# Performance work log

Measured on AMD Instinct MI355X. Metric: run time of the kernel, lower is better.

## Reference

```python
import jax, jax.numpy as jnp
import numpy as np

NUM_LAYERS = 2

def setup_inputs() -> dict:
    key = jax.random.key(0)
    ks = jax.random.split(key, 10)
    N, E, V, D, G = 50000, 800000, 100000, 128, 64
    node_ids = jax.random.randint(ks[0], (N,), 0, V)
    edge_index = jax.random.randint(ks[1], (2, E), 0, N)
    batch = jnp.sort(jax.random.randint(ks[2], (N,), 0, G))
    embed = jax.random.normal(ks[3], (V, D), dtype=jnp.float32)
    conv_w = jax.random.normal(ks[4], (NUM_LAYERS, D, D), dtype=jnp.float32) * (1.0 / np.sqrt(D))
    w_ih = jax.random.normal(ks[5], (3 * D, D), dtype=jnp.float32) * (1.0 / np.sqrt(D))
    w_hh = jax.random.normal(ks[6], (3 * D, D), dtype=jnp.float32) * (1.0 / np.sqrt(D))
    b_ih = jax.random.normal(ks[7], (3 * D,), dtype=jnp.float32) * 0.01
    b_hh = jax.random.normal(ks[8], (3 * D,), dtype=jnp.float32) * 0.01
    return {"node_ids": node_ids, "edge_index": edge_index, "batch": batch,
            "num_graphs": 64, "embed": embed, "conv_w": conv_w,
            "w_ih": w_ih, "w_hh": w_hh, "b_ih": b_ih, "b_hh": b_hh}


def _gru_cell(x, h, w_ih, w_hh, b_ih, b_hh):
    # torch.nn.GRUCell math; gate order r, z, n
    gi = x @ w_ih.T + b_ih
    gh = h @ w_hh.T + b_hh
    i_r, i_z, i_n = jnp.split(gi, 3, axis=-1)
    h_r, h_z, h_n = jnp.split(gh, 3, axis=-1)
    r = jax.nn.sigmoid(i_r + h_r)
    z = jax.nn.sigmoid(i_z + h_z)
    n = jnp.tanh(i_n + r * h_n)
    return (1.0 - z) * n + z * h


def reference(node_ids, edge_index, batch, num_graphs, embed, conv_w, w_ih, w_hh, b_ih, b_hh):
    N = node_ids.shape[0]
    src, dst = edge_index[0], edge_index[1]
    h = embed[node_ids]  # [N, D]
    for i in range(NUM_LAYERS):
        m = h @ conv_w[i]                                   # [N, D]
        agg = jax.ops.segment_sum(m[src], dst, num_segments=N)  # scatter-add messages
        h = _gru_cell(agg, h, w_ih, w_hh, b_ih, b_hh)
    # global mean pool per graph
    sums = jax.ops.segment_sum(h, batch, num_segments=num_graphs)       # [G, D]
    counts = jax.ops.segment_sum(jnp.ones((N,), h.dtype), batch, num_segments=num_graphs)
    return sums / jnp.maximum(counts, 1.0)[:, None]
```

## Files before the change

kernel.cpp:

```cpp
#include <hip/hip_runtime.h>
#include <hip/hip_bf16.h>


#define DTHREADS 256

typedef __attribute__((ext_vector_type(8))) short bf16x8;
typedef __attribute__((ext_vector_type(4))) float f32x4;

__device__ __forceinline__ float sigf(float x) { return 1.0f / (1.0f + __expf(-x)); }
__device__ __forceinline__ float tanhfast(float x) { return 1.0f - 2.0f / (1.0f + __expf(2.0f * x)); }

__device__ __forceinline__ unsigned short f2bf_rne(float x) {
  unsigned int u = __float_as_uint(x);
  u += 0x7fff + ((u >> 16) & 1);
  return (unsigned short)(u >> 16);
}
__device__ __forceinline__ float bf2f(unsigned int lo16) {
  return __uint_as_float(lo16 << 16);
}

__global__ __launch_bounds__(DTHREADS) void gather_kernel(
    const float* __restrict__ embed, const int* __restrict__ node_ids,
    unsigned short* __restrict__ hb, int N) {
  int idx = blockIdx.x * DTHREADS + threadIdx.x;
  if (idx >= N * 32) return;
  int n = idx >> 5;
  int c = (idx & 31) * 4;
  int v = node_ids[n];
  float4 val = *(const float4*)&embed[(size_t)v * 128 + c];
  unsigned short b[4] = {f2bf_rne(val.x), f2bf_rne(val.y), f2bf_rne(val.z), f2bf_rne(val.w)};
  *(ushort4*)&hb[(size_t)n * 128 + c] = *(ushort4*)b;
}

#define BSHIFT 7
#define BNODES 128

__global__ __launch_bounds__(DTHREADS) void bucket_hist_kernel(
    const int* __restrict__ dst, int* __restrict__ gcnt, int E, int NB) {
  __shared__ int lc[512];
  int tid = threadIdx.x;
  for (int i = tid; i < NB; i += DTHREADS) lc[i] = 0;
  __syncthreads();
  int base = blockIdx.x * 4096;
  #pragma unroll
  for (int q = 0; q < 16; ++q) {
    int e = base + q * 256 + tid;
    if (e < E) atomicAdd(&lc[dst[e] >> BSHIFT], 1);
  }
  __syncthreads();
  for (int i = tid; i < NB; i += DTHREADS) {
    int c = lc[i];
    if (c) atomicAdd(&gcnt[i], c);
  }
}

__global__ __launch_bounds__(512) void bucket_scan_kernel(
    const int* __restrict__ gcnt, int* __restrict__ ptr, int* __restrict__ cur,
    int* __restrict__ row_ptr, int NB, int N) {
  int tid = threadIdx.x;
  int lane = tid & 63, wv = tid >> 6;
  int v = (tid < NB) ? gcnt[tid] : 0;
  int x = v;
  #pragma unroll
  for (int off = 1; off < 64; off <<= 1) {
    int y = __shfl_up(x, (unsigned)off, 64);
    if (lane >= off) x += y;
  }
  __shared__ int ws[8];
  if (lane == 63) ws[wv] = x;
  __syncthreads();
  int woff = 0;
  for (int w = 0; w < wv; ++w) woff += ws[w];
  int excl = woff + x - v;
  if (tid < NB) { ptr[tid] = excl; cur[tid] = excl; }
  if (tid == 511) { int tot = woff + x; ptr[NB] = tot; row_ptr[N] = tot; }
}

__global__ __launch_bounds__(DTHREADS) void bucket_scatter_kernel(
    const int* __restrict__ src, const int* __restrict__ dst,
    int* __restrict__ cur, unsigned int* __restrict__ ebuf, int E, int NB) {
  __shared__ int lc[512];
  __shared__ int lbs[512];
  int tid = threadIdx.x;
  for (int i = tid; i < NB; i += DTHREADS) lc[i] = 0;
  __syncthreads();
  int base = blockIdx.x * 4096;
  int rank[16];
  #pragma unroll
  for (int q = 0; q < 16; ++q) {
    int e = base + q * 256 + tid;
    if (e < E) rank[q] = atomicAdd(&lc[dst[e] >> BSHIFT], 1);
  }
  __syncthreads();
  for (int i = tid; i < NB; i += DTHREADS) {
    int c = lc[i];
    lbs[i] = c ? atomicAdd(&cur[i], c) : 0;
  }
  __syncthreads();
  #pragma unroll
  for (int q = 0; q < 16; ++q) {
    int e = base + q * 256 + tid;
    if (e < E) {
      int d = dst[e];
      unsigned int pk = (unsigned int)src[e] | ((unsigned int)(d & (BNODES - 1)) << 17);
      ebuf[lbs[d >> BSHIFT] + rank[q]] = pk;
    }
  }
}

__global__ __launch_bounds__(DTHREADS) void bucket_sort_kernel(
    const unsigned int* __restrict__ ebuf, const int* __restrict__ ptr,
    int* __restrict__ row_ptr, int* __restrict__ csr_src, int N) {
  __shared__ int cnt[BNODES];
  __shared__ int sc[BNODES];
  const int tid = threadIdx.x;
  const int b = blockIdx.x;
  const int s = ptr[b], e = ptr[b + 1];
  if (tid < BNODES) cnt[tid] = 0;
  __syncthreads();
  for (int i = s + tid; i < e; i += DTHREADS)
    atomicAdd(&cnt[ebuf[i] >> 17], 1);
  __syncthreads();
  if (tid < BNODES) sc[tid] = cnt[tid];
  __syncthreads();
  #pragma unroll
  for (int off = 1; off < BNODES; off <<= 1) {
    int t = 0;
    if (tid < BNODES && tid >= off) t = sc[tid - off];
    __syncthreads();
    if (tid < BNODES) sc[tid] += t;
    __syncthreads();
  }
  if (tid < BNODES) {
    int excl = sc[tid] - cnt[tid];
    int n = b * BNODES + tid;
    if (n < N) row_ptr[n] = s + excl;
    cnt[tid] = excl;
  }
  __syncthreads();
  for (int i = s + tid; i < e; i += DTHREADS) {
    unsigned int pk = ebuf[i];
    int slot = atomicAdd(&cnt[pk >> 17], 1);
    csr_src[s + slot] = (int)(pk & 0x1FFFFu);
  }
}

__global__ __launch_bounds__(DTHREADS) void pack_w_kernel(
    const float* __restrict__ w, unsigned short* __restrict__ wpk, int J) {
  int f = blockIdx.x * DTHREADS + threadIdx.x;
  if (f >= J * 16) return;
  int l = f & 63;
  int s = (f >> 6) & 3;
  int t = (f >> 8) & 3;
  int jb = f >> 10;
  int j = jb * 64 + t * 16 + (l & 15);
  int kb = s * 32 + (l >> 4) * 8;
  unsigned short o[8];
  #pragma unroll
  for (int i = 0; i < 8; ++i) o[i] = f2bf_rne(w[j * 128 + kb + i]);
  *(uint4*)&wpk[(size_t)f * 8] = *(uint4*)o;
}

__global__ __launch_bounds__(DTHREADS) void pack_wc_kernel(
    const float* __restrict__ conv, const float* __restrict__ w_ih,
    unsigned short* __restrict__ wpk) {
  int id = blockIdx.x * DTHREADS + threadIdx.x;
  if (id >= 384 * 128) return;
  int f = id >> 3, i = id & 7;
  int l = f & 63;
  int s = (f >> 6) & 3;
  int t = (f >> 8) & 3;
  int jb = f >> 10;
  int j = jb * 64 + t * 16 + (l & 15);
  int k = s * 32 + (l >> 4) * 8 + i;
  float acc = 0.f;
  for (int d = 0; d < 128; d += 4) {
    float4 cv = *(const float4*)&conv[k * 128 + d];
    float4 wv = *(const float4*)&w_ih[j * 128 + d];
    acc += cv.x * wv.x + cv.y * wv.y + cv.z * wv.z + cv.w * wv.w;
  }
  wpk[(size_t)f * 8 + i] = f2bf_rne(acc);
}

__global__ __launch_bounds__(DTHREADS) void aggregate_kernel(
    const unsigned short* __restrict__ hb, const int* __restrict__ row_ptr,
    const int* __restrict__ csr_src, unsigned short* __restrict__ agg, int N) {
  int w = (blockIdx.x * DTHREADS + threadIdx.x) >> 6;
  if (w >= N) return;
  int lane = threadIdx.x & 63;
  int g = lane >> 4;
  int c = lane & 15;
  int s = row_ptr[w], e = row_ptr[w + 1];
  float acc[8] = {0.f, 0.f, 0.f, 0.f, 0.f, 0.f, 0.f, 0.f};
  for (int i = s; i < e; i += 16) {
    int idx[4]; bool vl[4]; uint4 d[4];
    #pragma unroll
    for (int q = 0; q < 4; ++q) {
      int ii = i + g + q * 4;
      vl[q] = ii < e;
      idx[q] = csr_src[vl[q] ? ii : s];
    }
    #pragma unroll
    for (int q = 0; q < 4; ++q)
      d[q] = *(const uint4*)&hb[(size_t)idx[q] * 128 + c * 8];
    #pragma unroll
    for (int q = 0; q < 4; ++q) {
      if (vl[q]) {
        const unsigned int* dp = (const unsigned int*)&d[q];
        #pragma unroll
        for (int k = 0; k < 4; ++k) {
          acc[2 * k]     += bf2f(dp[k] & 0xffffu);
          acc[2 * k + 1] += bf2f(dp[k] >> 16);
        }
      }
    }
  }
  #pragma unroll
  for (int q = 0; q < 8; ++q) acc[q] += __shfl_xor(acc[q], 16, 64);
  #pragma unroll
  for (int q = 0; q < 8; ++q) acc[q] += __shfl_xor(acc[q], 32, 64);
  if (g == 0) {
    unsigned int o[4];
    #pragma unroll
    for (int q = 0; q < 4; ++q)
      o[q] = (unsigned int)f2bf_rne(acc[2 * q]) | ((unsigned int)f2bf_rne(acc[2 * q + 1]) << 16);
    *(uint4*)&agg[(size_t)w * 128 + c * 8] = *(uint4*)o;
  }
}

__global__ __launch_bounds__(512, 2) void fused_gru_kernel(
    const unsigned short* __restrict__ aggb, const unsigned short* __restrict__ wpk_wc,
    const unsigned short* __restrict__ wpk_hh, const float* __restrict__ b_ih,
    const float* __restrict__ b_hh, unsigned short* __restrict__ hb,
    int N, int nchunks) {
  __shared__ __align__(16) unsigned short Ag[32 * 128];
  __shared__ __align__(16) unsigned short Hs[32 * 128];
  const int tid = threadIdx.x;
  const int wv = tid >> 6, lane = tid & 63;
  const int lm = lane & 15, quad = lane >> 4;

  bf16x8 BI[3][4], BH[3][4];
  #pragma unroll
  for (int g = 0; g < 3; ++g) {
    int jb = g * 2 + (wv >> 2);
    int t = wv & 3;
    #pragma unroll
    for (int s = 0; s < 4; ++s) {
      size_t f = ((size_t)(jb * 4 + t) * 4 + s) * 64 + lane;
      BI[g][s] = *(const bf16x8*)&wpk_wc[f * 8];
      BH[g][s] = *(const bf16x8*)&wpk_hh[f * 8];
    }
  }

  const int jc = wv * 16 + lm;
  const float bir = b_ih[jc], biz = b_ih[128 + jc], bin_ = b_ih[256 + jc];
  const float bhr = b_hh[jc], bhz = b_hh[128 + jc], bhn = b_hh[256 + jc];
  const int c0 = jc >> 3, ej = jc & 7;

  const int srow = tid >> 4, scol = tid & 15;
  const int sdc = (scol ^ (srow & 15)) * 8;

  int ci = blockIdx.x;
  uint4 va = make_uint4(0, 0, 0, 0), vh = make_uint4(0, 0, 0, 0);
  if (ci < nchunks) {
    int n = ci * 32 + srow;
    if (n < N) {
      va = *(const uint4*)&aggb[(size_t)n * 128 + scol * 8];
      vh = *(const uint4*)&hb[(size_t)n * 128 + scol * 8];
    }
  }

  for (; ci < nchunks; ci += gridDim.x) {
    *(uint4*)&Ag[srow * 128 + sdc] = va;
    *(uint4*)&Hs[srow * 128 + sdc] = vh;
    __syncthreads();

    int cn = ci + gridDim.x;
    va = make_uint4(0, 0, 0, 0); vh = make_uint4(0, 0, 0, 0);
    if (cn < nchunks) {
      int n = cn * 32 + srow;
      if (n < N) {
        va = *(const uint4*)&aggb[(size_t)n * 128 + scol * 8];
        vh = *(const uint4*)&hb[(size_t)n * 128 + scol * 8];
      }
    }

    f32x4 accI[2][3], accH[2][3];
    #pragma unroll
    for (int mi = 0; mi < 2; ++mi)
      #pragma unroll
      for (int g = 0; g < 3; ++g) {
        accI[mi][g] = (f32x4){0.f, 0.f, 0.f, 0.f};
        accH[mi][g] = (f32x4){0.f, 0.f, 0.f, 0.f};
      }

    #pragma unroll
    for (int s = 0; s < 4; ++s) {
      bf16x8 afA[2], afH[2];
      #pragma unroll
      for (int mi = 0; mi < 2; ++mi) {
        int m = mi * 16 + lm;
        int chunk = (s * 4 + quad) ^ (m & 15);
        afA[mi] = *(const bf16x8*)&Ag[m * 128 + chunk * 8];
        afH[mi] = *(const bf16x8*)&Hs[m * 128 + chunk * 8];
      }
      #pragma unroll
      for (int g = 0; g < 3; ++g)
        #pragma unroll
        for (int mi = 0; mi < 2; ++mi) {
          accI[mi][g] = __builtin_amdgcn_mfma_f32_16x16x32_bf16(afA[mi], BI[g][s], accI[mi][g], 0, 0, 0);
          accH[mi][g] = __builtin_amdgcn_mfma_f32_16x16x32_bf16(afH[mi], BH[g][s], accH[mi][g], 0, 0, 0);
        }
    }

    const int n0 = ci * 32;
    #pragma unroll
    for (int mi = 0; mi < 2; ++mi) {
      #pragma unroll
      for (int r = 0; r < 4; ++r) {
        int row = mi * 16 + quad * 4 + r;
        int n = n0 + row;
        if (n >= N) continue;
        float ir = accI[mi][0][r] + bir;
        float iz = accI[mi][1][r] + biz;
        float in_ = accI[mi][2][r] + bin_;
        float hr = accH[mi][0][r] + bhr;
        float hz = accH[mi][1][r] + bhz;
        float hn = accH[mi][2][r] + bhn;
        float rr = sigf(ir + hr);
        float zz = sigf(iz + hz);
        float nn = tanhfast(in_ + rr * hn);
        float hold = bf2f((unsigned int)Hs[row * 128 + ((c0 ^ (row & 15)) * 8) + ej]);
        hb[(size_t)n * 128 + jc] = f2bf_rne((1.f - zz) * nn + zz * hold);
      }
    }
    __syncthreads();
  }
}

__global__ __launch_bounds__(DTHREADS) void pool1_kernel(
    const unsigned short* __restrict__ hb, const int* __restrict__ batch,
    float* __restrict__ outsum, int N) {
  int b = blockIdx.x;
  int c = threadIdx.x & 127;
  int half = threadIdx.x >> 7;
  int nbeg = b * 64;
  int nend = min(nbeg + 64, N);
  float acc = 0.f;
  int cur = -1;
  for (int n = nbeg + half; n < nend; n += 2) {
    int g = batch[n];
    if (g != cur) {
      if (cur >= 0) atomicAdd(&outsum[(size_t)cur * 128 + c], acc);
      acc = 0.f;
      cur = g;
    }
    acc += bf2f((unsigned int)hb[(size_t)n * 128 + c]);
  }
  if (cur >= 0) atomicAdd(&outsum[(size_t)cur * 128 + c], acc);
}

__device__ __forceinline__ int lbound(const int* a, int n, int key) {
  int lo = 0, hi = n;
  while (lo < hi) {
    int mid = (lo + hi) >> 1;
    if (a[mid] < key) lo = mid + 1; else hi = mid;
  }
  return lo;
}

__global__ __launch_bounds__(128) void pool2_kernel(
    const float* __restrict__ outsum, const int* __restrict__ batch,
    float* __restrict__ out, int N) {
  int g = blockIdx.x;
  int c = threadIdx.x;
  int lo = lbound(batch, N, g);
  int hi = lbound(batch, N, g + 1);
  out[(size_t)g * 128 + c] = outsum[(size_t)g * 128 + c] / (float)max(hi - lo, 1);
}

extern "C" void kernel_launch(void* const* d_in, const int* in_sizes, int n_in,
                              void* d_out, int out_size, void* d_ws, size_t ws_size,
                              hipStream_t stream) {
  const int* node_ids = (const int*)d_in[0];
  const int* edge_index = (const int*)d_in[1];
  const int* batch = (const int*)d_in[2];
  const float* embed = (const float*)d_in[4];
  const float* conv_w = (const float*)d_in[5];
  const float* w_ih = (const float*)d_in[6];
  const float* w_hh = (const float*)d_in[7];
  const float* b_ih = (const float*)d_in[8];
  const float* b_hh = (const float*)d_in[9];
  float* out = (float*)d_out;

  const int N = in_sizes[0];
  const int E = in_sizes[1] / 2;
  const int G = out_size / 128;
  const int NUM_LAYERS = in_sizes[5] / (128 * 128);
  const int NB = (N + BNODES - 1) >> BSHIFT;

  const int* e_src = edge_index;
  const int* e_dst = edge_index + E;

  char* p = (char*)d_ws;
  unsigned short* hb = (unsigned short*)p;    p += (size_t)N * 128 * 2;
  unsigned short* aggb = (unsigned short*)p;  p += (size_t)N * 128 * 2;
  float* outsum = (float*)p;                  p += (size_t)G * 128 * 4;
  unsigned short* wpk_hh = (unsigned short*)p; p += (size_t)384 * 128 * 2;
  unsigned short* wpk_wc = (unsigned short*)p; p += (size_t)NUM_LAYERS * 384 * 128 * 2;
  int* bkt_cnt = (int*)p;  p += 512 * 4;
  int* bkt_ptr = (int*)p;  p += 513 * 4;
  int* bkt_cur = (int*)p;  p += 512 * 4;
  int* row_ptr = (int*)p;  p += (size_t)(N + 1) * 4;
  unsigned int* ebuf = (unsigned int*)p;  p += (size_t)E * 4;
  int* csr_src = (int*)p;  p += (size_t)E * 4;

  const int nEB = (E + 4095) / 4096;

  hipMemsetAsync(bkt_cnt, 0, 512 * sizeof(int), stream);
  hipMemsetAsync(outsum, 0, (size_t)G * 128 * sizeof(float), stream);

  bucket_hist_kernel<<<nEB, DTHREADS, 0, stream>>>(e_dst, bkt_cnt, E, NB);
  bucket_scan_kernel<<<1, 512, 0, stream>>>(bkt_cnt, bkt_ptr, bkt_cur, row_ptr, NB, N);
  bucket_scatter_kernel<<<nEB, DTHREADS, 0, stream>>>(e_src, e_dst, bkt_cur, ebuf, E, NB);
  bucket_sort_kernel<<<NB, DTHREADS, 0, stream>>>(ebuf, bkt_ptr, row_ptr, csr_src, N);

  pack_w_kernel<<<(384 * 16 + DTHREADS - 1) / DTHREADS, DTHREADS, 0, stream>>>(w_hh, wpk_hh, 384);
  for (int L = 0; L < NUM_LAYERS; ++L)
    pack_wc_kernel<<<(384 * 128 + DTHREADS - 1) / DTHREADS, DTHREADS, 0, stream>>>(
        conv_w + (size_t)L * 128 * 128, w_ih, wpk_wc + (size_t)L * 384 * 128);

  gather_kernel<<<(N * 32 + DTHREADS - 1) / DTHREADS, DTHREADS, 0, stream>>>(embed, node_ids, hb, N);

  const int nchunks = (N + 31) / 32;
  for (int L = 0; L < NUM_LAYERS; ++L) {
    aggregate_kernel<<<((size_t)N * 64 + DTHREADS - 1) / DTHREADS, DTHREADS, 0, stream>>>(
        hb, row_ptr, csr_src, aggb, N);
    fused_gru_kernel<<<256, 512, 0, stream>>>(
        aggb, wpk_wc + (size_t)L * 384 * 128, wpk_hh, b_ih, b_hh, hb, N, nchunks);
  }

  pool1_kernel<<<(N + 63) / 64, DTHREADS, 0, stream>>>(hb, batch, outsum, N);
  pool2_kernel<<<G, 128, 0, stream>>>(outsum, batch, out, N);
}
```

Before: 296.5 us.

## Merge weight packing launches, fold outsum memset into scan, double GRU grid

Combines the w_hh pack and per-layer conv·w_ih pack kernels into one launch, and moves the outsum zeroing into the single-block bucket scan kernel so the memset call goes away. This is meant to cut per-launch overhead on the short preprocessing path. Separately, the fused GRU kernel grid goes from 256 to 512 blocks to raise parallelism, though that may add per-block weight loading overhead.

Measured after the change: 292.9 us. No clear change (-1.2%).

```diff
diff --git a/kernel.cpp b/kernel.cpp
--- a/kernel.cpp
+++ b/kernel.cpp
@@ -3,6 +3,8 @@
 
 
 #define DTHREADS 256
+#define BSHIFT 7
+#define BNODES 128
 
 typedef __attribute__((ext_vector_type(8))) short bf16x8;
 typedef __attribute__((ext_vector_type(4))) float f32x4;
@@ -32,9 +34,6 @@
   *(ushort4*)&hb[(size_t)n * 128 + c] = *(ushort4*)b;
 }
 
-#define BSHIFT 7
-#define BNODES 128
-
 __global__ __launch_bounds__(DTHREADS) void bucket_hist_kernel(
     const int* __restrict__ dst, int* __restrict__ gcnt, int E, int NB) {
   __shared__ int lc[512];
@@ -56,8 +55,9 @@
 
 __global__ __launch_bounds__(512) void bucket_scan_kernel(
     const int* __restrict__ gcnt, int* __restrict__ ptr, int* __restrict__ cur,
-    int* __restrict__ row_ptr, int NB, int N) {
+    int* __restrict__ row_ptr, float* __restrict__ outsum, int osz, int NB, int N) {
   int tid = threadIdx.x;
+  for (int i = tid; i < osz; i += 512) outsum[i] = 0.f;
   int lane = tid & 63, wv = tid >> 6;
   int v = (tid < NB) ? gcnt[tid] : 0;
   int x = v;
@@ -145,41 +145,38 @@
   }
 }
 
-__global__ __launch_bounds__(DTHREADS) void pack_w_kernel(
-    const float* __restrict__ w, unsigned short* __restrict__ wpk, int J) {
-  int f = blockIdx.x * DTHREADS + threadIdx.x;
-  if (f >= J * 16) return;
-  int l = f & 63;
-  int s = (f >> 6) & 3;
-  int t = (f >> 8) & 3;
-  int jb = f >> 10;
-  int j = jb * 64 + t * 16 + (l & 15);
-  int kb = s * 32 + (l >> 4) * 8;
-  unsigned short o[8];
-  #pragma unroll
-  for (int i = 0; i < 8; ++i) o[i] = f2bf_rne(w[j * 128 + kb + i]);
-  *(uint4*)&wpk[(size_t)f * 8] = *(uint4*)o;
-}
-
-__global__ __launch_bounds__(DTHREADS) void pack_wc_kernel(
-    const float* __restrict__ conv, const float* __restrict__ w_ih,
-    unsigned short* __restrict__ wpk) {
+__global__ __launch_bounds__(DTHREADS) void pack_all_kernel(
+    const float* __restrict__ w_hh, const float* __restrict__ conv_w,
+    const float* __restrict__ w_ih, unsigned short* __restrict__ wpk_hh,
+    unsigned short* __restrict__ wpk_wc, int nl) {
   int id = blockIdx.x * DTHREADS + threadIdx.x;
-  if (id >= 384 * 128) return;
-  int f = id >> 3, i = id & 7;
+  int seg = id / (384 * 128);
+  if (seg > nl) return;
+  int r = id - seg * (384 * 128);
+  int f = r >> 3, i = r & 7;
   int l = f & 63;
   int s = (f >> 6) & 3;
   int t = (f >> 8) & 3;
   int jb = f >> 10;
   int j = jb * 64 + t * 16 + (l & 15);
   int k = s * 32 + (l >> 4) * 8 + i;
-  float acc = 0.f;
-  for (int d = 0; d < 128; d += 4) {
-    float4 cv = *(const float4*)&conv[k * 128 + d];
-    float4 wv = *(const float4*)&w_ih[j * 128 + d];
-    acc += cv.x * wv.x + cv.y * wv.y + cv.z * wv.z + cv.w * wv.w;
-  }
-  wpk[(size_t)f * 8 + i] = f2bf_rne(acc);
+  float val;
+  unsigned short* dst;
+  if (seg == 0) {
+    val = w_hh[j * 128 + k];
+    dst = wpk_hh;
+  } else {
+    const float* conv = conv_w + (size_t)(seg - 1) * 128 * 128;
+    float acc = 0.f;
+    for (int d = 0; d < 128; d += 4) {
+      float4 cv = *(const float4*)&conv[k * 128 + d];
+      float4 wv = *(const float4*)&w_ih[j * 128 + d];
+      acc += cv.x * wv.x + cv.y * wv.y + cv.z * wv.z + cv.w * wv.w;
+    }
+    val = acc;
+    dst = wpk_wc + (size_t)(seg - 1) * 384 * 128;
+  }
+  dst[(size_t)f * 8 + i] = f2bf_rne(val);
 }
 
 __global__ __launch_bounds__(DTHREADS) void aggregate_kernel(
@@ -418,17 +415,18 @@
   const int nEB = (E + 4095) / 4096;
 
   hipMemsetAsync(bkt_cnt, 0, 512 * sizeof(int), stream);
-  hipMemsetAsync(outsum, 0, (size_t)G * 128 * sizeof(float), stream);
 
   bucket_hist_kernel<<<nEB, DTHREADS, 0, stream>>>(e_dst, bkt_cnt, E, NB);
-  bucket_scan_kernel<<<1, 512, 0, stream>>>(bkt_cnt, bkt_ptr, bkt_cur, row_ptr, NB, N);
+  bucket_scan_kernel<<<1, 512, 0, stream>>>(bkt_cnt, bkt_ptr, bkt_cur, row_ptr,
+                                            outsum, G * 128, NB, N);
   bucket_scatter_kernel<<<nEB, DTHREADS, 0, stream>>>(e_src, e_dst, bkt_cur, ebuf, E, NB);
   bucket_sort_kernel<<<NB, DTHREADS, 0, stream>>>(ebuf, bkt_ptr, row_ptr, csr_src, N);
 
-  pack_w_kernel<<<(384 * 16 + DTHREADS - 1) / DTHREADS, DTHREADS, 0, stream>>>(w_hh, wpk_hh, 384);
-  for (int L = 0; L < NUM_LAYERS; ++L)
-    pack_wc_kernel<<<(384 * 128 + DTHREADS - 1) / DTHREADS, DTHREADS, 0, stream>>>(
-        conv_w + (size_t)L * 128 * 128, w_ih, wpk_wc + (size_t)L * 384 * 128);
+  {
+    int total = (NUM_LAYERS + 1) * 384 * 128;
+    pack_all_kernel<<<(total + DTHREADS - 1) / DTHREADS, DTHREADS, 0, stream>>>(
+        w_hh, conv_w, w_ih, wpk_hh, wpk_wc, NUM_LAYERS);
+  }
 
   gather_kernel<<<(N * 32 + DTHREADS - 1) / DTHREADS, DTHREADS, 0, stream>>>(embed, node_ids, hb, N);
 
@@ -436,7 +434,7 @@
   for (int L = 0; L < NUM_LAYERS; ++L) {
     aggregate_kernel<<<((size_t)N * 64 + DTHREADS - 1) / DTHREADS, DTHREADS, 0, stream>>>(
         hb, row_ptr, csr_src, aggb, N);
-    fused_gru_kernel<<<256, 512, 0, stream>>>(
+    fused_gru_kernel<<<512, 512, 0, stream>>>(
         aggb, wpk_wc + (size_t)L * 384 * 128, wpk_hh, b_ih, b_hh, hb, N, nchunks);
   }
 
```
